# Performance work log

Measured on AMD Instinct MI355X. Metric: run time of the kernel, lower is better.

The kernel has to match this reference:

```python
import jax, jax.numpy as jnp
import numpy as np

NUM_REL = 7
EPS = 1e-5
N, E = 30000, 480000
D_IN, D_H = 21, 512


def _bn(x, g, b):
    # BatchNorm1d over nodes (training-mode batch statistics, biased var like torch)
    mu = x.mean(axis=0)
    var = x.var(axis=0)
    return (x - mu) * jax.lax.rsqrt(var + EPS) * g + b


def _conv(x, src, seg_idx, lin_w, lin_b, self_w, self_b, bn_g, bn_b):
    # GeometricRelationalGraphConv: gather src features, scatter-add per (dst, relation)
    d = x.shape[1]
    msg = x[src]                                                   # (E, d)
    upd = jax.ops.segment_sum(msg, seg_idx, num_segments=N * NUM_REL)
    upd = upd.reshape(N, NUM_REL * d)                              # (N, 7*d)
    out = upd @ lin_w.T + lin_b + x @ self_w.T + self_b            # linear + self-loop
    out = _bn(out, bn_g, bn_b)                                     # conv-internal BN
    return jax.nn.relu(out)


def setup_inputs() -> dict:
    key = jax.random.key(0)
    ks = jax.random.split(key, 16)
    inp = {
        "x": jax.random.normal(ks[0], (N, D_IN), dtype=jnp.float32),
        "src": jax.random.randint(ks[1], (E,), 0, N, dtype=jnp.int32),
        "dst": jax.random.randint(ks[2], (E,), 0, N, dtype=jnp.int32),
        "rel": jax.random.randint(ks[3], (E,), 0, NUM_REL, dtype=jnp.int32),
    }
    dims = [(D_IN, D_H), (D_H, D_H), (D_H, D_H)]
    k = 4
    for i, (din, dout) in enumerate(dims):
        inp[f"lin_w{i}"] = jax.random.normal(ks[k], (dout, NUM_REL * din), dtype=jnp.float32) * 0.05
        inp[f"self_w{i}"] = jax.random.normal(ks[k + 1], (dout, din), dtype=jnp.float32) * 0.05
        k += 2
        inp[f"lin_b{i}"] = jnp.zeros((dout,), jnp.float32)
        inp[f"self_b{i}"] = jnp.zeros((dout,), jnp.float32)
        inp[f"bn1_g{i}"] = jnp.ones((dout,), jnp.float32)
        inp[f"bn1_b{i}"] = jnp.zeros((dout,), jnp.float32)
        inp[f"bn2_g{i}"] = jnp.ones((dout,), jnp.float32)
        inp[f"bn2_b{i}"] = jnp.zeros((dout,), jnp.float32)
    return inp


def reference(x, src, dst, rel,
              lin_w0, lin_b0, self_w0, self_b0, bn1_g0, bn1_b0, bn2_g0, bn2_b0,
              lin_w1, lin_b1, self_w1, self_b1, bn1_g1, bn1_b1, bn2_g1, bn2_b1,
              lin_w2, lin_b2, self_w2, self_b2, bn1_g2, bn1_b2, bn2_g2, bn2_b2):
    seg_idx = dst * NUM_REL + rel                                  # (E,)
    layers = [
        (lin_w0, lin_b0, self_w0, self_b0, bn1_g0, bn1_b0, bn2_g0, bn2_b0),
        (lin_w1, lin_b1, self_w1, self_b1, bn1_g1, bn1_b1, bn2_g1, bn2_b1),
        (lin_w2, lin_b2, self_w2, self_b2, bn1_g2, bn1_b2, bn2_g2, bn2_b2),
    ]
    hiddens = []
    h = x
    for lw, lb, sw, sb, g1, b1, g2, b2 in layers:
        h = _conv(h, src, seg_idx, lw, lb, sw, sb, g1, b1)
        h = _bn(h, g2, b2)                                         # GearNet outer BN
        hiddens.append(h)
    return jnp.concatenate(hiddens, axis=-1)                      # (N, 3*512) concat_hidden
```

## Files before the change

### kernel.cpp

```cpp
#include <hip/hip_runtime.h>

#define NN   30000
#define NE   480000
#define NR   7
#define NSEG (NN*NR)
#define DH   512
#define DIN  21
#define EPSB 1e-5f
#define BK   32
#define KSEG 3584
#define CHMAX 15360

typedef __attribute__((ext_vector_type(8))) short bf16x8;
typedef __attribute__((ext_vector_type(8))) unsigned short u16x8;
typedef __attribute__((ext_vector_type(4))) float f32x4;
typedef unsigned short ushortT;

static inline size_t align256(size_t x){ return (x + 255) & ~(size_t)255; }

__device__ inline float bf2f(ushortT u){
    unsigned int i = ((unsigned int)u) << 16; float f; __builtin_memcpy(&f, &i, 4); return f;
}
__device__ inline ushortT f2bf(float f){
    unsigned int i; __builtin_memcpy(&i, &f, 4);
    unsigned int r = i + 0x7FFFu + ((i >> 16) & 1u);
    return (ushortT)(r >> 16);
}

__device__ inline void load_lds16(const ushortT* g, ushortT* l){
    __builtin_amdgcn_global_load_lds((const __attribute__((address_space(1))) unsigned int*)g,
                                     (__attribute__((address_space(3))) unsigned int*)l,
                                     16, 0, 0);
}


__global__ void hist_k(const int* __restrict__ dst, const int* __restrict__ rel,
                       int* __restrict__ counts){
    int e = blockIdx.x*256 + threadIdx.x;
    if (e < NE) atomicAdd(&counts[dst[e]*NR + rel[e]], 1);
}

__global__ void scan1_k(const int* __restrict__ counts, int* __restrict__ bsum){
    __shared__ int sd[256];
    int t = threadIdx.x;
    int base = blockIdx.x*1024 + t*4;
    int s = 0;
#pragma unroll
    for (int i = 0; i < 4; i++){ int idx = base + i; if (idx < NSEG) s += counts[idx]; }
    sd[t] = s; __syncthreads();
    for (int off = 128; off > 0; off >>= 1){
        if (t < off) sd[t] += sd[t+off];
        __syncthreads();
    }
    if (t == 0) bsum[blockIdx.x] = sd[0];
}

__global__ void scan2_k(int* __restrict__ bsum, int nb, int* __restrict__ seg_start){
    __shared__ int sd[256];
    int t = threadIdx.x;
    int v = (t < nb) ? bsum[t] : 0;
    sd[t] = v; __syncthreads();
    for (int off = 1; off < 256; off <<= 1){
        int x = sd[t];
        if (t >= off) x += sd[t-off];
        __syncthreads();
        sd[t] = x; __syncthreads();
    }
    if (t < nb) bsum[t] = (t == 0) ? 0 : sd[t-1];
    if (t == 0) seg_start[NSEG] = NE;
}

__global__ void scan3_k(const int* __restrict__ counts, const int* __restrict__ bsum,
                        int* __restrict__ seg_start){
    __shared__ int sd[256];
    int t = threadIdx.x;
    int base = blockIdx.x*1024 + t*4;
    int v[4]; int s = 0;
#pragma unroll
    for (int i = 0; i < 4; i++){ int idx = base + i; v[i] = (idx < NSEG) ? counts[idx] : 0; s += v[i]; }
    sd[t] = s; __syncthreads();
    for (int off = 1; off < 256; off <<= 1){
        int x = sd[t];
        if (t >= off) x += sd[t-off];
        __syncthreads();
        sd[t] = x; __syncthreads();
    }
    int excl = sd[t] - s + bsum[blockIdx.x];
#pragma unroll
    for (int i = 0; i < 4; i++){
        int idx = base + i;
        if (idx < NSEG){ seg_start[idx] = excl; excl += v[i]; }
    }
}

__global__ void scatter_k(const int* __restrict__ src, const int* __restrict__ dst,
                          const int* __restrict__ rel, const int* __restrict__ seg_start,
                          int* __restrict__ cursor, int* __restrict__ src_sorted){
    int e = blockIdx.x*256 + threadIdx.x;
    if (e < NE){
        int s = dst[e]*NR + rel[e];
        int pos = seg_start[s] + atomicAdd(&cursor[s], 1);
        src_sorted[pos] = src[e];
    }
}


__global__ void segsum21b_k(const float* __restrict__ x0,
                            const int* __restrict__ seg_start, const int* __restrict__ src_sorted,
                            ushortT* __restrict__ Acat){
    int n = blockIdx.x;
    int t = threadIdx.x;
    ushortT* arow = Acat + (long)n*192;
    if (t < DIN){
        int sb = n*NR;
        int e0 = seg_start[sb];
#pragma unroll
        for (int r = 0; r < NR; r++){
            int e1 = seg_start[sb + r + 1];
            float a = 0.f;
            for (int e = e0; e < e1; e++) a += x0[(long)src_sorted[e]*DIN + t];
            e0 = e1;
            arow[r*DIN + t] = f2bf(a);
        }
        arow[7*DIN + t] = f2bf(x0[(long)n*DIN + t]);
    }
    if (t >= 40) arow[168 + (t - 40)] = 0;
}


__global__ __launch_bounds__(256)
void segsum_wave_k(const ushortT* __restrict__ hbf,
                   const int* __restrict__ seg_start, const int* __restrict__ src_sorted,
                   ushortT* __restrict__ Acat, int c0, int cn){
    int wid = (blockIdx.x*256 + threadIdx.x) >> 6;
    if (wid >= cn) return;
    const int n = c0 + wid;
    const int lane = (threadIdx.x & 63);
    const int co = lane*8;

    int sb[8];
#pragma unroll
    for (int i = 0; i < 8; i++) sb[i] = seg_start[n*NR + i];

    ushortT* arow = Acat + (long)wid*KSEG + co;
#pragma unroll
    for (int r = 0; r < NR; r++){
        float a[8];
#pragma unroll
        for (int j = 0; j < 8; j++) a[j] = 0.f;
        int e = sb[r], e1 = sb[r+1];
        for (; e + 1 < e1; e += 2){
            u16x8 v0 = *reinterpret_cast<const u16x8*>(hbf + (long)src_sorted[e]*DH + co);
            u16x8 v1 = *reinterpret_cast<const u16x8*>(hbf + (long)src_sorted[e+1]*DH + co);
#pragma unroll
            for (int j = 0; j < 8; j++) a[j] += bf2f((ushortT)v0[j]) + bf2f((ushortT)v1[j]);
        }
        if (e < e1){
            u16x8 v = *reinterpret_cast<const u16x8*>(hbf + (long)src_sorted[e]*DH + co);
#pragma unroll
            for (int j = 0; j < 8; j++) a[j] += bf2f((ushortT)v[j]);
        }
        u16x8 o;
#pragma unroll
        for (int j = 0; j < 8; j++) o[j] = f2bf(a[j]);
        *reinterpret_cast<u16x8*>(arow + r*DH) = o;
    }
}


__global__ void convw_k(const float* __restrict__ lw, const float* __restrict__ sw,
                        int d, int Kp, ushortT* __restrict__ Wc){
    int i = blockIdx.x*256 + threadIdx.x;
    if (i < DH*Kp){
        int n = i / Kp, k = i % Kp;
        float v;
        if (k < 7*d)      v = lw[(long)n*7*d + k];
        else if (k < 8*d) v = sw[(long)n*d + (k - 7*d)];
        else              v = 0.f;
        Wc[i] = f2bf(v);
    }
}


__global__ __launch_bounds__(256)
void gemm_mfma_k(const ushortT* __restrict__ A, int lda, int ntA,
                 const ushortT* __restrict__ hbase, int M,
                 const ushortT* __restrict__ W, int ldw,
                 const float* __restrict__ b1, const float* __restrict__ b2,
                 float* __restrict__ C, int nt, float* __restrict__ sums){
    __shared__ ushortT As[3][128*BK];
    __shared__ ushortT Bs[3][128*BK];
    const int t    = threadIdx.x;

    const int nwg = gridDim.x;
    int q = nwg >> 3, rmd = nwg & 7;
    int xcd = blockIdx.x & 7, slot = blockIdx.x >> 3;
    int l = xcd*q + min(xcd, rmd) + slot;
    const int bm = (l >> 2)*128;
    const int bn = (l & 3)*128;

    const int w    = t >> 6;
    const int lane = t & 63;

    int f0 = w*128 + lane, f1 = f0 + 64;
    const int ar0 = min(bm + (f0 >> 2), M-1), ac0 = (f0 & 3)*8;
    const int ar1 = min(bm + (f1 >> 2), M-1), ac1 = (f1 & 3)*8;
    const int br0 = bn + (f0 >> 2), br1 = bn + (f1 >> 2);
    const int d0 = (w*128 +  0)*8;
    const int d1 = (w*128 + 64)*8;

    f32x4 acc[4][4];
#pragma unroll
    for (int m = 0; m < 4; m++)
#pragma unroll
        for (int n = 0; n < 4; n++) acc[m][n] = (f32x4){0.f,0.f,0.f,0.f};

    const int wm = w >> 1, wn = w & 1;
    const int r = lane & 15, hi = lane >> 4;

    auto stage = [&](int kt, int b){
        const ushortT* p0;
        const ushortT* p1;
        if (kt < ntA){
            p0 = A + (long)ar0*lda + kt*BK + ac0;
            p1 = A + (long)ar1*lda + kt*BK + ac1;
        } else {
            int k0 = (kt - ntA)*BK;
            p0 = hbase + (long)ar0*DH + k0 + ac0;
            p1 = hbase + (long)ar1*DH + k0 + ac1;
        }
        load_lds16(p0, &As[b][d0]);
        load_lds16(p1, &As[b][d1]);
        load_lds16(W + (long)br0*ldw + kt*BK + ac0, &Bs[b][d0]);
        load_lds16(W + (long)br1*ldw + kt*BK + ac1, &Bs[b][d1]);
    };

    stage(0, 0);
    stage(1, 1);

    for (int kt = 0; kt < nt; ++kt){
        if (kt + 1 < nt) asm volatile("s_waitcnt vmcnt(4)" ::: "memory");
        else             asm volatile("s_waitcnt vmcnt(0)" ::: "memory");
        __builtin_amdgcn_s_barrier();
        __builtin_amdgcn_sched_barrier(0);
        if (kt + 2 < nt) stage(kt + 2, (kt + 2) % 3);
        const int buf = kt % 3;
        bf16x8 af[4], bfr[4];
#pragma unroll
        for (int m = 0; m < 4; m++)
            af[m] = *reinterpret_cast<const bf16x8*>(&As[buf][(wm*64 + m*16 + r)*BK + hi*8]);
#pragma unroll
        for (int n = 0; n < 4; n++)
            bfr[n] = *reinterpret_cast<const bf16x8*>(&Bs[buf][(wn*64 + n*16 + r)*BK + hi*8]);
#pragma unroll
        for (int m = 0; m < 4; m++)
#pragma unroll
            for (int n = 0; n < 4; n++)
                acc[m][n] = __builtin_amdgcn_mfma_f32_16x16x32_bf16(af[m], bfr[n], acc[m][n], 0, 0, 0);
    }

#pragma unroll
    for (int n = 0; n < 4; n++){
        int col = bn + wn*64 + n*16 + r;
        float bb = b1[col] + b2[col];
        float s = 0.f, s2 = 0.f;
#pragma unroll
        for (int m = 0; m < 4; m++){
            int row = bm + wm*64 + m*16 + hi*4;
#pragma unroll
            for (int q2 = 0; q2 < 4; q2++){
                if (row + q2 < M){
                    float v = acc[m][n][q2] + bb;
                    C[(long)(row + q2)*DH + col] = v;
                    s += v; s2 = fmaf(v, v, s2);
                }
            }
        }
        s  += __shfl_xor(s, 16);  s  += __shfl_xor(s, 32);
        s2 += __shfl_xor(s2, 16); s2 += __shfl_xor(s2, 32);
        if (hi == 0){
            atomicAdd(&sums[col], s);
            atomicAdd(&sums[DH + col], s2);
        }
    }
}


__global__ void finalize_k(const float* __restrict__ sums, const float* __restrict__ g,
                           const float* __restrict__ b, float* __restrict__ ac){
    int c = blockIdx.x*256 + threadIdx.x;
    if (c < DH){
        float mu  = sums[c] * (1.f/NN);
        float var = sums[DH + c] * (1.f/NN) - mu*mu;
        var = fmaxf(var, 0.f);
        float a = g[c] * rsqrtf(var + EPSB);
        ac[c]      = a;
        ac[DH + c] = fmaf(-mu, a, b[c]);
    }
}

__global__ void bnrelu_k(float* __restrict__ buf, int M, const float* __restrict__ ac,
                         float* __restrict__ sums2){
    int col = blockIdx.x*256 + threadIdx.x;
    int r0 = blockIdx.y*128;
    int r1 = min(r0 + 128, M);
    float a = ac[col], c = ac[DH + col];
    float s = 0.f, s2 = 0.f;
    for (int r = r0; r < r1; r++){
        long idx = (long)r*DH + col;
        float y = fmaxf(fmaf(a, buf[idx], c), 0.f);
        buf[idx] = y;
        s += y; s2 = fmaf(y, y, s2);
    }
    atomicAdd(&sums2[col], s);
    atomicAdd(&sums2[DH + col], s2);
}

__global__ void bn2write_k(const float* __restrict__ buf, const float* __restrict__ ac,
                           float* __restrict__ out, ushortT* __restrict__ hbf, int layer){
    long i = (long)blockIdx.x*256 + threadIdx.x;
    if (i < (long)NN*DH){
        int r = (int)(i >> 9);
        int c = (int)(i & 511);
        float h = fmaf(ac[c], buf[i], ac[DH + c]);
        out[(long)r*(3*DH) + layer*DH + c] = h;
        hbf[i] = f2bf(h);
    }
}


extern "C" void kernel_launch(void* const* d_in, const int* in_sizes, int n_in,
                              void* d_out, int out_size, void* d_ws, size_t ws_size,
                              hipStream_t stream){
    const float* x0  = (const float*)d_in[0];
    const int*   src = (const int*)d_in[1];
    const int*   dst = (const int*)d_in[2];
    const int*   rel = (const int*)d_in[3];
    const float* lin_w[3]  = {(const float*)d_in[4],  (const float*)d_in[12], (const float*)d_in[20]};
    const float* self_w[3] = {(const float*)d_in[5],  (const float*)d_in[13], (const float*)d_in[21]};
    const float* lin_b[3]  = {(const float*)d_in[6],  (const float*)d_in[14], (const float*)d_in[22]};
    const float* self_b[3] = {(const float*)d_in[7],  (const float*)d_in[15], (const float*)d_in[23]};
    const float* bn1_g[3]  = {(const float*)d_in[8],  (const float*)d_in[16], (const float*)d_in[24]};
    const float* bn1_b[3]  = {(const float*)d_in[9],  (const float*)d_in[17], (const float*)d_in[25]};
    const float* bn2_g[3]  = {(const float*)d_in[10], (const float*)d_in[18], (const float*)d_in[26]};
    const float* bn2_b[3]  = {(const float*)d_in[11], (const float*)d_in[19], (const float*)d_in[27]};

    char* ws = (char*)d_ws;
    size_t off = 0;
    auto alloc = [&](size_t bytes)->char*{ char* p = ws + off; off = align256(off + bytes); return p; };

    int*     counts     = (int*)alloc((size_t)NSEG*4);
    int*     cursor     = (int*)alloc((size_t)NSEG*4);
    int*     seg_start  = (int*)alloc((size_t)(NSEG+1)*4);
    int*     bsum       = (int*)alloc(1024*4);
    int*     src_sorted = (int*)alloc((size_t)NE*4);
    float*   stats      = (float*)alloc((size_t)8*DH*4);
    float*   sums1 = stats;            float* sums2 = stats + 2*DH;
    float*   ac1   = stats + 4*DH;     float* ac2   = stats + 6*DH;
    float*   outbuf = (float*)alloc((size_t)NN*DH*4);
    ushortT* hbf    = (ushortT*)alloc((size_t)NN*DH*2);
    ushortT* Wcat   = (ushortT*)alloc((size_t)DH*4096*2);
    ushortT* Acat0  = (ushortT*)alloc((size_t)NN*192*2);

    size_t remain = (ws_size > off) ? (ws_size - off) : 0;
    long max_nodes = (long)(remain / ((size_t)KSEG*2));
    int chunk = (int)((max_nodes > CHMAX) ? CHMAX : max_nodes);
    chunk &= ~127;
    if (chunk < 128) chunk = 128;
    ushortT* Acat = (ushortT*)(ws + off);

    hipMemsetAsync(counts, 0, (size_t)NSEG*4, stream);
    hipMemsetAsync(cursor, 0, (size_t)NSEG*4, stream);
    hist_k<<<(NE+255)/256, 256, 0, stream>>>(dst, rel, counts);
    int nb = (NSEG + 1023)/1024;
    scan1_k<<<nb, 256, 0, stream>>>(counts, bsum);
    scan2_k<<<1, 256, 0, stream>>>(bsum, nb, seg_start);
    scan3_k<<<nb, 256, 0, stream>>>(counts, bsum, seg_start);
    scatter_k<<<(NE+255)/256, 256, 0, stream>>>(src, dst, rel, seg_start, cursor, src_sorted);

    const int MB = (NN + 127)/128;

    for (int layer = 0; layer < 3; layer++){
        int d  = (layer == 0) ? DIN : DH;
        int Kp = (layer == 0) ? 192 : 8*DH;
        convw_k<<<(DH*Kp + 255)/256, 256, 0, stream>>>(lin_w[layer], self_w[layer], d, Kp, Wcat);
        hipMemsetAsync(stats, 0, (size_t)4*DH*4, stream);

        if (layer == 0){
            segsum21b_k<<<NN, 64, 0, stream>>>(x0, seg_start, src_sorted, Acat0);
            gemm_mfma_k<<<MB*4, 256, 0, stream>>>(
                Acat0, 192, 6, Acat0, NN, Wcat, 192,
                lin_b[layer], self_b[layer], outbuf, 6, sums1);
        } else {
            for (int c0 = 0; c0 < NN; c0 += chunk){
                int cn = (NN - c0 < chunk) ? (NN - c0) : chunk;
                segsum_wave_k<<<(cn + 3)/4, 256, 0, stream>>>(
                    hbf, seg_start, src_sorted, Acat, c0, cn);
                gemm_mfma_k<<<((cn + 127)/128)*4, 256, 0, stream>>>(
                    Acat, KSEG, 112, hbf + (long)c0*DH, cn, Wcat, 4096,
                    lin_b[layer], self_b[layer],
                    outbuf + (long)c0*DH, 128, sums1);
            }
        }

        finalize_k<<<2, 256, 0, stream>>>(sums1, bn1_g[layer], bn1_b[layer], ac1);
        bnrelu_k<<<dim3(2, (NN+127)/128), 256, 0, stream>>>(outbuf, NN, ac1, sums2);
        finalize_k<<<2, 256, 0, stream>>>(sums2, bn2_g[layer], bn2_b[layer], ac2);
        bn2write_k<<<((long)NN*DH + 255)/256, 256, 0, stream>>>(outbuf, ac2, (float*)d_out, hbf, layer);
    }
}
```

Measured before the change: 959.5 us.

## Enlarge GEMM tile to 256 rows, store conv output in bf16, unroll segsum

The GEMM now runs 512-thread workgroups covering 256x128 tiles, so each W tile loaded into LDS serves twice as many rows. The intermediate conv output buffer changes from fp32 to bf16, which halves traffic in the BN/ReLU passes, and the BN statistics are taken from the rounded values. The segment-sum gather is unrolled to four edges per iteration, and the chunk cap is raised to the full node count so fewer chunked launches are needed. The risks are extra precision loss from storing pre-BN activations in bf16, and higher register and LDS pressure that may lower occupancy.

```diff
diff --git a/kernel.cpp b/kernel.cpp
--- a/kernel.cpp
+++ b/kernel.cpp
@@ -9,7 +9,6 @@
 #define EPSB 1e-5f
 #define BK   32
 #define KSEG 3584
-#define CHMAX 15360
 
 typedef __attribute__((ext_vector_type(8))) short bf16x8;
 typedef __attribute__((ext_vector_type(8))) unsigned short u16x8;
@@ -149,13 +148,17 @@
 #pragma unroll
         for (int j = 0; j < 8; j++) a[j] = 0.f;
         int e = sb[r], e1 = sb[r+1];
-        for (; e + 1 < e1; e += 2){
-            u16x8 v0 = *reinterpret_cast<const u16x8*>(hbf + (long)src_sorted[e]*DH + co);
+        for (; e + 3 < e1; e += 4){
+            u16x8 v0 = *reinterpret_cast<const u16x8*>(hbf + (long)src_sorted[e  ]*DH + co);
             u16x8 v1 = *reinterpret_cast<const u16x8*>(hbf + (long)src_sorted[e+1]*DH + co);
-#pragma unroll
-            for (int j = 0; j < 8; j++) a[j] += bf2f((ushortT)v0[j]) + bf2f((ushortT)v1[j]);
-        }
-        if (e < e1){
+            u16x8 v2 = *reinterpret_cast<const u16x8*>(hbf + (long)src_sorted[e+2]*DH + co);
+            u16x8 v3 = *reinterpret_cast<const u16x8*>(hbf + (long)src_sorted[e+3]*DH + co);
+#pragma unroll
+            for (int j = 0; j < 8; j++)
+                a[j] += (bf2f((ushortT)v0[j]) + bf2f((ushortT)v1[j]))
+                      + (bf2f((ushortT)v2[j]) + bf2f((ushortT)v3[j]));
+        }
+        for (; e < e1; e++){
             u16x8 v = *reinterpret_cast<const u16x8*>(hbf + (long)src_sorted[e]*DH + co);
 #pragma unroll
             for (int j = 0; j < 8; j++) a[j] += bf2f((ushortT)v[j]);
@@ -182,39 +185,36 @@
 }
 
 
-__global__ __launch_bounds__(256)
+__global__ __launch_bounds__(512)
 void gemm_mfma_k(const ushortT* __restrict__ A, int lda, int ntA,
                  const ushortT* __restrict__ hbase, int M,
                  const ushortT* __restrict__ W, int ldw,
                  const float* __restrict__ b1, const float* __restrict__ b2,
-                 float* __restrict__ C, int nt, float* __restrict__ sums){
-    __shared__ ushortT As[3][128*BK];
+                 ushortT* __restrict__ C, int nt, float* __restrict__ sums){
+    __shared__ ushortT As[3][256*BK];
     __shared__ ushortT Bs[3][128*BK];
-    const int t    = threadIdx.x;
+    const int t = threadIdx.x;
 
     const int nwg = gridDim.x;
     int q = nwg >> 3, rmd = nwg & 7;
     int xcd = blockIdx.x & 7, slot = blockIdx.x >> 3;
     int l = xcd*q + min(xcd, rmd) + slot;
-    const int bm = (l >> 2)*128;
+    const int bm = (l >> 2)*256;
     const int bn = (l & 3)*128;
 
-    const int w    = t >> 6;
+    const int ar0 = min(bm + (t >> 2), M-1);
+    const int ar1 = min(bm + 128 + (t >> 2), M-1);
+    const int brw = bn + (t >> 2);
+    const int acu = (t & 3)*8;
+
+    f32x4 acc[4][4];
+#pragma unroll
+    for (int m = 0; m < 4; m++)
+#pragma unroll
+        for (int n = 0; n < 4; n++) acc[m][n] = (f32x4){0.f,0.f,0.f,0.f};
+
+    const int w = t >> 6;
     const int lane = t & 63;
-
-    int f0 = w*128 + lane, f1 = f0 + 64;
-    const int ar0 = min(bm + (f0 >> 2), M-1), ac0 = (f0 & 3)*8;
-    const int ar1 = min(bm + (f1 >> 2), M-1), ac1 = (f1 & 3)*8;
-    const int br0 = bn + (f0 >> 2), br1 = bn + (f1 >> 2);
-    const int d0 = (w*128 +  0)*8;
-    const int d1 = (w*128 + 64)*8;
-
-    f32x4 acc[4][4];
-#pragma unroll
-    for (int m = 0; m < 4; m++)
-#pragma unroll
-        for (int n = 0; n < 4; n++) acc[m][n] = (f32x4){0.f,0.f,0.f,0.f};
-
     const int wm = w >> 1, wn = w & 1;
     const int r = lane & 15, hi = lane >> 4;
 
@@ -222,24 +222,23 @@
         const ushortT* p0;
         const ushortT* p1;
         if (kt < ntA){
-            p0 = A + (long)ar0*lda + kt*BK + ac0;
-            p1 = A + (long)ar1*lda + kt*BK + ac1;
+            p0 = A + (long)ar0*lda + kt*BK + acu;
+            p1 = A + (long)ar1*lda + kt*BK + acu;
         } else {
             int k0 = (kt - ntA)*BK;
-            p0 = hbase + (long)ar0*DH + k0 + ac0;
-            p1 = hbase + (long)ar1*DH + k0 + ac1;
-        }
-        load_lds16(p0, &As[b][d0]);
-        load_lds16(p1, &As[b][d1]);
-        load_lds16(W + (long)br0*ldw + kt*BK + ac0, &Bs[b][d0]);
-        load_lds16(W + (long)br1*ldw + kt*BK + ac1, &Bs[b][d1]);
+            p0 = hbase + (long)ar0*DH + k0 + acu;
+            p1 = hbase + (long)ar1*DH + k0 + acu;
+        }
+        load_lds16(p0, &As[b][t*8]);
+        load_lds16(p1, &As[b][(t + 512)*8]);
+        load_lds16(W + (long)brw*ldw + kt*BK + acu, &Bs[b][t*8]);
     };
 
     stage(0, 0);
     stage(1, 1);
 
     for (int kt = 0; kt < nt; ++kt){
-        if (kt + 1 < nt) asm volatile("s_waitcnt vmcnt(4)" ::: "memory");
+        if (kt + 1 < nt) asm volatile("s_waitcnt vmcnt(3)" ::: "memory");
         else             asm volatile("s_waitcnt vmcnt(0)" ::: "memory");
         __builtin_amdgcn_s_barrier();
         __builtin_amdgcn_sched_barrier(0);
@@ -270,9 +269,10 @@
 #pragma unroll
             for (int q2 = 0; q2 < 4; q2++){
                 if (row + q2 < M){
-                    float v = acc[m][n][q2] + bb;
-                    C[(long)(row + q2)*DH + col] = v;
-                    s += v; s2 = fmaf(v, v, s2);
+                    ushortT u = f2bf(acc[m][n][q2] + bb);
+                    C[(long)(row + q2)*DH + col] = u;
+                    float vr = bf2f(u);
+                    s += vr; s2 = fmaf(vr, vr, s2);
                 }
             }
         }
@@ -299,7 +299,7 @@
     }
 }
 
-__global__ void bnrelu_k(float* __restrict__ buf, int M, const float* __restrict__ ac,
+__global__ void bnrelu_k(ushortT* __restrict__ buf, int M, const float* __restrict__ ac,
                          float* __restrict__ sums2){
     int col = blockIdx.x*256 + threadIdx.x;
     int r0 = blockIdx.y*128;
@@ -308,21 +308,23 @@
     float s = 0.f, s2 = 0.f;
     for (int r = r0; r < r1; r++){
         long idx = (long)r*DH + col;
-        float y = fmaxf(fmaf(a, buf[idx], c), 0.f);
-        buf[idx] = y;
-        s += y; s2 = fmaf(y, y, s2);
+        float y = fmaxf(fmaf(a, bf2f(buf[idx]), c), 0.f);
+        ushortT u = f2bf(y);
+        buf[idx] = u;
+        float yr = bf2f(u);
+        s += yr; s2 = fmaf(yr, yr, s2);
     }
     atomicAdd(&sums2[col], s);
     atomicAdd(&sums2[DH + col], s2);
 }
 
-__global__ void bn2write_k(const float* __restrict__ buf, const float* __restrict__ ac,
+__global__ void bn2write_k(const ushortT* __restrict__ buf, const float* __restrict__ ac,
                            float* __restrict__ out, ushortT* __restrict__ hbf, int layer){
     long i = (long)blockIdx.x*256 + threadIdx.x;
     if (i < (long)NN*DH){
         int r = (int)(i >> 9);
         int c = (int)(i & 511);
-        float h = fmaf(ac[c], buf[i], ac[DH + c]);
+        float h = fmaf(ac[c], bf2f(buf[i]), ac[DH + c]);
         out[(long)r*(3*DH) + layer*DH + c] = h;
         hbf[i] = f2bf(h);
     }
@@ -357,16 +359,16 @@
     float*   stats      = (float*)alloc((size_t)8*DH*4);
     float*   sums1 = stats;            float* sums2 = stats + 2*DH;
     float*   ac1   = stats + 4*DH;     float* ac2   = stats + 6*DH;
-    float*   outbuf = (float*)alloc((size_t)NN*DH*4);
+    ushortT* outbuf = (ushortT*)alloc((size_t)NN*DH*2);
     ushortT* hbf    = (ushortT*)alloc((size_t)NN*DH*2);
     ushortT* Wcat   = (ushortT*)alloc((size_t)DH*4096*2);
     ushortT* Acat0  = (ushortT*)alloc((size_t)NN*192*2);
 
     size_t remain = (ws_size > off) ? (ws_size - off) : 0;
     long max_nodes = (long)(remain / ((size_t)KSEG*2));
-    int chunk = (int)((max_nodes > CHMAX) ? CHMAX : max_nodes);
-    chunk &= ~127;
-    if (chunk < 128) chunk = 128;
+    int chunk = (int)((max_nodes > NN) ? NN : max_nodes);
+    chunk &= ~255;
+    if (chunk < 256) chunk = 256;
     ushortT* Acat = (ushortT*)(ws + off);
 
     hipMemsetAsync(counts, 0, (size_t)NSEG*4, stream);
@@ -378,8 +380,6 @@
     scan3_k<<<nb, 256, 0, stream>>>(counts, bsum, seg_start);
     scatter_k<<<(NE+255)/256, 256, 0, stream>>>(src, dst, rel, seg_start, cursor, src_sorted);
 
-    const int MB = (NN + 127)/128;
-
     for (int layer = 0; layer < 3; layer++){
         int d  = (layer == 0) ? DIN : DH;
         int Kp = (layer == 0) ? 192 : 8*DH;
@@ -388,7 +388,7 @@
 
         if (layer == 0){
             segsum21b_k<<<NN, 64, 0, stream>>>(x0, seg_start, src_sorted, Acat0);
-            gemm_mfma_k<<<MB*4, 256, 0, stream>>>(
+            gemm_mfma_k<<<((NN + 255)/256)*4, 512, 0, stream>>>(
                 Acat0, 192, 6, Acat0, NN, Wcat, 192,
                 lin_b[layer], self_b[layer], outbuf, 6, sums1);
         } else {
@@ -396,7 +396,7 @@
                 int cn = (NN - c0 < chunk) ? (NN - c0) : chunk;
                 segsum_wave_k<<<(cn + 3)/4, 256, 0, stream>>>(
                     hbf, seg_start, src_sorted, Acat, c0, cn);
-                gemm_mfma_k<<<((cn + 127)/128)*4, 256, 0, stream>>>(
+                gemm_mfma_k<<<((cn + 255)/256)*4, 512, 0, stream>>>(
                     Acat, KSEG, 112, hbf + (long)c0*DH, cn, Wcat, 4096,
                     lin_b[layer], self_b[layer],
                     outbuf + (long)c0*DH, 128, sums1);
```

Result: slower. 1.136 ms (+18.4%).
